# Kernel optimization log

Hardware: AMD Instinct MI355X
Metric: run time of the kernel (lower is better)

## Reference

```python
import jax, jax.numpy as jnp
import numpy as np

N_NODES = 1048576
N_SEG = 16384
NODES_PER_SEG = N_NODES // N_SEG
D = 128
EPS = 1e-5


def setup_inputs() -> dict:
    key = jax.random.key(0)
    ks = jax.random.split(key, 8)
    feat = jax.random.normal(ks[0], (N_NODES, D), dtype=jnp.float32)
    position_weight = jax.random.uniform(ks[1], (N_NODES,), dtype=jnp.float32)
    # equal-size segments (sessions): contiguous, sorted segment ids
    segment_ids = jnp.repeat(jnp.arange(N_SEG, dtype=jnp.int32), NODES_PER_SEG)
    # last node of each segment
    last_nodes = jnp.arange(N_SEG, dtype=jnp.int32) * NODES_PER_SEG + (NODES_PER_SEG - 1)
    # parameters
    gamma = jnp.ones((D,), dtype=jnp.float32)
    beta = jnp.zeros((D,), dtype=jnp.float32)
    s = 1.0 / np.sqrt(D)
    W_u = jax.random.uniform(ks[2], (D, D), dtype=jnp.float32, minval=-s, maxval=s)
    W_i = jax.random.uniform(ks[3], (D, D), dtype=jnp.float32, minval=-s, maxval=s)
    b_i = jax.random.uniform(ks[4], (D,), dtype=jnp.float32, minval=-s, maxval=s)
    w_e = jax.random.uniform(ks[5], (D,), dtype=jnp.float32, minval=-s, maxval=s)
    return {
        "feat": feat, "position_weight": position_weight,
        "last_nodes": last_nodes, "segment_ids": segment_ids,
        "gamma": gamma, "beta": beta, "W_u": W_u, "W_i": W_i,
        "b_i": b_i, "w_e": w_e, "num_segments": N_SEG,
    }


def reference(feat, position_weight, last_nodes, segment_ids, gamma, beta,
              W_u, W_i, b_i, w_e, num_segments):
    # BatchNorm1d (training-mode batch statistics)
    mean = feat.mean(axis=0)
    var = jnp.mean((feat - mean) ** 2, axis=0)
    f = (feat - mean) * (gamma / jnp.sqrt(var + EPS)) + beta  # [N, D]

    feat_u = f @ W_u.T                                         # [N, H]
    feat_last = f[last_nodes] @ W_i.T + b_i                    # [B, H]
    # broadcast_nodes: gather per-graph vector back to its nodes
    e = jax.nn.sigmoid(feat_u + feat_last[segment_ids]) @ w_e  # [N]

    # segment softmax over nodes of each graph
    m = jax.ops.segment_max(e, segment_ids, num_segments=num_segments)
    ex = jnp.exp(e - m[segment_ids])
    denom = jax.ops.segment_sum(ex, segment_ids, num_segments=num_segments)
    alpha = ex / denom[segment_ids]                            # [N]

    rst = jax.ops.segment_sum(f * alpha[:, None], segment_ids,
                              num_segments=num_segments)       # [B, D]
    position_rst = jax.ops.segment_sum(f * position_weight[:, None], segment_ids,
                                       num_segments=num_segments)  # [B, D]
    return rst, position_rst
```

## Files before the change

### kernel.cpp

```cpp
#include <hip/hip_runtime.h>

#define N_NODES 1048576
#define N_SEG   16384
#define NPS     64
#define D       128
#define EPS     1e-5f

typedef float f4 __attribute__((ext_vector_type(4)));
typedef float f32x4 __attribute__((ext_vector_type(4)));
typedef __bf16 bf16x8 __attribute__((ext_vector_type(8)));
typedef unsigned u32x4 __attribute__((ext_vector_type(4)));

__global__ __launch_bounds__(256) void k_stats(const float* __restrict__ feat,
                                               float* __restrict__ part) {
    int t = threadIdx.x;
    long gid = (long)blockIdx.x * 256 + t;
    const f4* f4p = (const f4*)feat;
    f4 s = {0.f,0.f,0.f,0.f}, q = {0.f,0.f,0.f,0.f};
#pragma unroll 8
    for (int k = 0; k < 64; ++k) {
        f4 v = f4p[gid + (long)k * 524288];
        s += v;
        q += v * v;
    }
    __shared__ f4 red[2][8][32];
    red[0][t >> 5][t & 31] = s;
    red[1][t >> 5][t & 31] = q;
    __syncthreads();
    int stat = t >> 7, c = t & 127;
    const float* base = (const float*)&red[stat][0][0];
    float acc = 0.f;
#pragma unroll
    for (int r = 0; r < 8; ++r) acc += base[r * 128 + c];
    part[(stat * 128 + c) * 2048 + blockIdx.x] = acc;
}

__global__ __launch_bounds__(256) void k_scale(const float* __restrict__ part,
                                               const float* __restrict__ gamma,
                                               const float* __restrict__ beta,
                                               float* __restrict__ scl,
                                               float* __restrict__ shf) {
    int t = threadIdx.x, c = blockIdx.x;
    float s1 = 0.f, s2 = 0.f;
#pragma unroll
    for (int j = 0; j < 8; ++j) {
        s1 += part[c * 2048 + t + 256 * j];
        s2 += part[(128 + c) * 2048 + t + 256 * j];
    }
    __shared__ float rs[256], rq[256];
    rs[t] = s1; rq[t] = s2;
    __syncthreads();
    for (int off = 128; off > 0; off >>= 1) {
        if (t < off) { rs[t] += rs[t + off]; rq[t] += rq[t + off]; }
        __syncthreads();
    }
    if (t == 0) {
        float mean = rs[0] / (float)N_NODES;
        float var  = rq[0] / (float)N_NODES - mean * mean;
        float sc   = gamma[c] * rsqrtf(var + EPS);
        scl[c] = sc;
        shf[c] = beta[c] - mean * sc;
    }
}

__device__ inline unsigned pk2(float x, float y) {
    unsigned a = __builtin_bit_cast(unsigned, x);
    unsigned b = __builtin_bit_cast(unsigned, y);
    a = (a + 0x7fffu + ((a >> 16) & 1u)) >> 16;
    b = (b + 0x7fffu + ((b >> 16) & 1u)) & 0xffff0000u;
    return a | b;
}
__device__ inline bf16x8 lds8(const unsigned short* p, int row, int kb) {
    int addr = (row * 256 + kb) ^ ((row & 7) << 4);
    return *(const bf16x8*)((const char*)p + addr);
}
__device__ inline bf16x8 bfrag(const float* __restrict__ W, int h, int kk, int g4) {
    const float* p = W + h * 128 + kk * 32 + g4 * 8;
    f4 u = *(const f4*)p;
    f4 v = *(const f4*)(p + 4);
    u32x4 r = { pk2(u.x, u.y), pk2(u.z, u.w), pk2(v.x, v.y), pk2(v.z, v.w) };
    return __builtin_bit_cast(bf16x8, r);
}
__device__ inline void bar_lgkm() {
    asm volatile("s_waitcnt lgkmcnt(0)" ::: "memory");
    __builtin_amdgcn_s_barrier();
    __builtin_amdgcn_sched_barrier(0);
}
__device__ inline void bar_vm1() {
    asm volatile("s_waitcnt vmcnt(1) lgkmcnt(0)" ::: "memory");
    __builtin_amdgcn_s_barrier();
    __builtin_amdgcn_sched_barrier(0);
}
__device__ inline void bar_vm0() {
    asm volatile("s_waitcnt vmcnt(0) lgkmcnt(0)" ::: "memory");
    __builtin_amdgcn_s_barrier();
    __builtin_amdgcn_sched_barrier(0);
}
__device__ inline void stage_tile(const float* __restrict__ segbase, float* fbuf,
                                  int w, int lane) {
#pragma unroll
    for (int j = 0; j < 8; ++j) {
        int chunk = w * 8 + j;
        int p = (chunk << 10) + lane * 16;
        int g = p ^ (((p >> 9) & 7) << 4);
        __builtin_amdgcn_global_load_lds(
            (const __attribute__((address_space(1))) void*)((const char*)segbase + g),
            (__attribute__((address_space(3))) void*)((char*)fbuf + (chunk << 10)),
            16, 0, 0);
    }
}

__global__ __launch_bounds__(256, 2) void k_main(const float* __restrict__ feat,
                                                 const float* __restrict__ pw,
                                                 const float* __restrict__ Wu,
                                                 const float* __restrict__ Wi,
                                                 const float* __restrict__ bi,
                                                 const float* __restrict__ we,
                                                 const float* __restrict__ scl,
                                                 const float* __restrict__ shf,
                                                 float* __restrict__ out) {
    __shared__ __align__(16) float fbuf[64 * 128];
    __shared__ __align__(16) unsigned short abuf[64 * 128];
    __shared__ float flp_s[8][128];
    __shared__ float pw_s[512];
    __shared__ float epart[4][64];
    __shared__ float wpR[4][128];
    __shared__ float wpP[4][128];

    int t = threadIdx.x;
    int lane = t & 63, w = t >> 6;
    int l15 = lane & 15, g4 = lane >> 4;
    int c0 = 4 * (t & 31);
    f4 vscl = *(const f4*)(scl + c0);
    f4 vshf = *(const f4*)(shf + c0);
    int h_a = l15 + 32 * w;
    int h_b = h_a + 16;
    int seg0 = blockIdx.x * 8;

    stage_tile(feat + (long)seg0 * NPS * D, fbuf, w, lane);
    pw_s[t] = pw[seg0 * NPS + t];
    pw_s[t + 256] = pw[seg0 * NPS + t + 256];
    {
        int r = t >> 5;
        long row = (long)(seg0 + r) * NPS + (NPS - 1);
        f4 v = *(const f4*)(feat + row * 128 + c0);
        v = v * vscl + vshf;
        int addr = (r * 256 + 8 * (t & 31)) ^ ((r & 7) << 4);
        *(uint2*)((char*)abuf + addr) = make_uint2(pk2(v.x, v.y), pk2(v.z, v.w));
        int r2 = r + 8;
        int addr2 = (r2 * 256 + 8 * (t & 31)) ^ ((r2 & 7) << 4);
        *(uint2*)((char*)abuf + addr2) = make_uint2(0u, 0u);
    }
    bar_lgkm();
    {
        f32x4 a2[2];
        a2[0] = (f32x4){0.f,0.f,0.f,0.f};
        a2[1] = (f32x4){0.f,0.f,0.f,0.f};
#pragma unroll
        for (int kk = 0; kk < 4; ++kk) {
            bf16x8 a = lds8(abuf, l15, kk * 64 + g4 * 16);
            a2[0] = __builtin_amdgcn_mfma_f32_16x16x32_bf16(a, bfrag(Wi, h_a, kk, g4), a2[0], 0, 0, 0);
            a2[1] = __builtin_amdgcn_mfma_f32_16x16x32_bf16(a, bfrag(Wi, h_b, kk, g4), a2[1], 0, 0, 0);
        }
        float bia = bi[h_a], bib = bi[h_b];
#pragma unroll
        for (int r = 0; r < 4; ++r) {
            int si = 4 * g4 + r;
            if (si < 8) {
                flp_s[si][h_a] = a2[0][r] + bia;
                flp_s[si][h_b] = a2[1][r] + bib;
            }
        }
    }
    bf16x8 bW[8];
#pragma unroll
    for (int kk = 0; kk < 4; ++kk) {
        bW[kk]     = bfrag(Wu, h_a, kk, g4);
        bW[4 + kk] = bfrag(Wu, h_b, kk, g4);
    }
    float we0 = we[h_a], we1 = we[h_b];
    bar_vm0();

    for (int it = 0; it < 8; ++it) {
        int seg = seg0 + it;
#pragma unroll
        for (int k = 0; k < 8; ++k) {
            int n = (t >> 5) + 8 * k;
            int q = (n * 512 + 16 * (t & 31)) ^ ((n & 7) << 4);
            f4 v = *(const f4*)((const char*)fbuf + q);
            v = v * vscl + vshf;
            int addr = (n * 256 + 8 * (t & 31)) ^ ((n & 7) << 4);
            *(uint2*)((char*)abuf + addr) = make_uint2(pk2(v.x, v.y), pk2(v.z, v.w));
        }
        bar_lgkm();
        if (it < 7)
            stage_tile(feat + (long)(seg + 1) * NPS * D, fbuf, w, lane);

        float fl0 = flp_s[it][h_a];
        float fl1 = flp_s[it][h_b];
        f32x4 acc[4][2];
#pragma unroll
        for (int nf = 0; nf < 4; ++nf) {
            acc[nf][0] = (f32x4){0.f,0.f,0.f,0.f};
            acc[nf][1] = (f32x4){0.f,0.f,0.f,0.f};
        }
#pragma unroll
        for (int kk = 0; kk < 4; ++kk) {
            int kb = kk * 64 + g4 * 16;
            bf16x8 a[4];
#pragma unroll
            for (int nf = 0; nf < 4; ++nf) a[nf] = lds8(abuf, l15 + 16 * nf, kb);
#pragma unroll
            for (int nf = 0; nf < 4; ++nf) {
                acc[nf][0] = __builtin_amdgcn_mfma_f32_16x16x32_bf16(a[nf], bW[kk],     acc[nf][0], 0, 0, 0);
                acc[nf][1] = __builtin_amdgcn_mfma_f32_16x16x32_bf16(a[nf], bW[4 + kk], acc[nf][1], 0, 0, 0);
            }
        }
#pragma unroll
        for (int nf = 0; nf < 4; ++nf) {
#pragma unroll
            for (int r = 0; r < 4; ++r) {
                float x0 = acc[nf][0][r] + fl0;
                float x1 = acc[nf][1][r] + fl1;
                float p = we0 / (1.f + __expf(-x0)) + we1 / (1.f + __expf(-x1));
                p += __shfl_xor(p, 1);
                p += __shfl_xor(p, 2);
                p += __shfl_xor(p, 4);
                p += __shfl_xor(p, 8);
                if (l15 == 0) epart[w][16 * nf + 4 * g4 + r] = p;
            }
        }
        bar_lgkm();

        float e = epart[0][lane] + epart[1][lane] + epart[2][lane] + epart[3][lane];
        float m = e;
#pragma unroll
        for (int off = 32; off > 0; off >>= 1) m = fmaxf(m, __shfl_xor(m, off));
        float ex = __expf(e - m);
        float sd = ex;
#pragma unroll
        for (int off = 32; off > 0; off >>= 1) sd += __shfl_xor(sd, off);
        float al = ex / sd;

        f4 racc = {0.f,0.f,0.f,0.f}, pacc = {0.f,0.f,0.f,0.f};
#pragma unroll
        for (int k = 0; k < 8; ++k) {
            int n = (t >> 5) + 8 * k;
            int addr = (n * 256 + 8 * (t & 31)) ^ ((n & 7) << 4);
            uint2 u = *(const uint2*)((const char*)abuf + addr);
            f4 fv;
            fv.x = __builtin_bit_cast(float, u.x << 16);
            fv.y = __builtin_bit_cast(float, u.x & 0xffff0000u);
            fv.z = __builtin_bit_cast(float, u.y << 16);
            fv.w = __builtin_bit_cast(float, u.y & 0xffff0000u);
            float av = __shfl(al, n);
            float pv = pw_s[it * NPS + n];
            racc += av * fv;
            pacc += pv * fv;
        }
#pragma unroll
        for (int c = 0; c < 4; ++c) {
            racc[c] += __shfl_xor(racc[c], 32);
            pacc[c] += __shfl_xor(pacc[c], 32);
        }
        if (lane < 32) {
            *(f4*)&wpR[w][4 * lane] = racc;
            *(f4*)&wpP[w][4 * lane] = pacc;
        }
        bar_lgkm();

        if (t < 128) {
            out[(long)seg * 128 + t] = wpR[0][t] + wpR[1][t] + wpR[2][t] + wpR[3][t];
        } else {
            int c = t - 128;
            out[(long)N_SEG * 128 + (long)seg * 128 + c] =
                wpP[0][c] + wpP[1][c] + wpP[2][c] + wpP[3][c];
        }
        bar_vm1();
    }
}

extern "C" void kernel_launch(void* const* d_in, const int* in_sizes, int n_in,
                              void* d_out, int out_size, void* d_ws, size_t ws_size,
                              hipStream_t stream) {
    const float* feat       = (const float*)d_in[0];
    const float* pw         = (const float*)d_in[1];
    const float* gamma      = (const float*)d_in[4];
    const float* beta       = (const float*)d_in[5];
    const float* Wu         = (const float*)d_in[6];
    const float* Wi         = (const float*)d_in[7];
    const float* bi         = (const float*)d_in[8];
    const float* we         = (const float*)d_in[9];
    float* out = (float*)d_out;

    float* ws   = (float*)d_ws;
    float* part = ws;
    float* wscl = ws + 524288;
    float* wshf = ws + 524288 + 128;

    k_stats<<<dim3(2048), dim3(256), 0, stream>>>(feat, part);
    k_scale<<<dim3(128),  dim3(256), 0, stream>>>(part, gamma, beta, wscl, wshf);
    k_main <<<dim3(2048), dim3(256), 0, stream>>>(feat, pw, Wu, Wi, bi, we, wscl, wshf, out);
}
```

Measured before the change: 359.9 us.

## Prefetch next segment tile into registers instead of async global-to-LDS staging

Replaces the global_load_lds staging of each 64x128 fp32 segment tile into a shared buffer with direct register prefetch: each thread loads 8 float4 values for the next segment while the current one is computed, then normalizes and packs them into the bf16 LDS tile. This removes the 32KB fp32 LDS buffer and its read-back, lowering LDS traffic and footprint, and drops the vmcnt-based barriers. In exchange it raises VGPR pressure by 32 registers, which may limit occupancy under launch_bounds(256,2), and the loads' latency is hidden only by the compiler's waitcnt placement.

```diff
diff --git a/kernel.cpp b/kernel.cpp
--- a/kernel.cpp
+++ b/kernel.cpp
@@ -82,32 +82,10 @@
     return __builtin_bit_cast(bf16x8, r);
 }
 __device__ inline void bar_lgkm() {
+    __builtin_amdgcn_sched_barrier(0);
     asm volatile("s_waitcnt lgkmcnt(0)" ::: "memory");
     __builtin_amdgcn_s_barrier();
     __builtin_amdgcn_sched_barrier(0);
-}
-__device__ inline void bar_vm1() {
-    asm volatile("s_waitcnt vmcnt(1) lgkmcnt(0)" ::: "memory");
-    __builtin_amdgcn_s_barrier();
-    __builtin_amdgcn_sched_barrier(0);
-}
-__device__ inline void bar_vm0() {
-    asm volatile("s_waitcnt vmcnt(0) lgkmcnt(0)" ::: "memory");
-    __builtin_amdgcn_s_barrier();
-    __builtin_amdgcn_sched_barrier(0);
-}
-__device__ inline void stage_tile(const float* __restrict__ segbase, float* fbuf,
-                                  int w, int lane) {
-#pragma unroll
-    for (int j = 0; j < 8; ++j) {
-        int chunk = w * 8 + j;
-        int p = (chunk << 10) + lane * 16;
-        int g = p ^ (((p >> 9) & 7) << 4);
-        __builtin_amdgcn_global_load_lds(
-            (const __attribute__((address_space(1))) void*)((const char*)segbase + g),
-            (__attribute__((address_space(3))) void*)((char*)fbuf + (chunk << 10)),
-            16, 0, 0);
-    }
 }
 
 __global__ __launch_bounds__(256, 2) void k_main(const float* __restrict__ feat,
@@ -119,7 +97,6 @@
                                                  const float* __restrict__ scl,
                                                  const float* __restrict__ shf,
                                                  float* __restrict__ out) {
-    __shared__ __align__(16) float fbuf[64 * 128];
     __shared__ __align__(16) unsigned short abuf[64 * 128];
     __shared__ float flp_s[8][128];
     __shared__ float pw_s[512];
@@ -137,7 +114,14 @@
     int h_b = h_a + 16;
     int seg0 = blockIdx.x * 8;
 
-    stage_tile(feat + (long)seg0 * NPS * D, fbuf, w, lane);
+    f4 fn[8];
+    {
+        const f4* src = (const f4*)(feat + (long)seg0 * NPS * D);
+#pragma unroll
+        for (int k = 0; k < 8; ++k) fn[k] = src[t + 256 * k];
+    }
+    __builtin_amdgcn_sched_barrier(0);
+
     pw_s[t] = pw[seg0 * NPS + t];
     pw_s[t + 256] = pw[seg0 * NPS + t + 256];
     {
@@ -179,22 +163,24 @@
         bW[4 + kk] = bfrag(Wu, h_b, kk, g4);
     }
     float we0 = we[h_a], we1 = we[h_b];
-    bar_vm0();
+    bar_lgkm();
 
     for (int it = 0; it < 8; ++it) {
         int seg = seg0 + it;
 #pragma unroll
         for (int k = 0; k < 8; ++k) {
+            f4 v = fn[k] * vscl + vshf;
             int n = (t >> 5) + 8 * k;
-            int q = (n * 512 + 16 * (t & 31)) ^ ((n & 7) << 4);
-            f4 v = *(const f4*)((const char*)fbuf + q);
-            v = v * vscl + vshf;
             int addr = (n * 256 + 8 * (t & 31)) ^ ((n & 7) << 4);
             *(uint2*)((char*)abuf + addr) = make_uint2(pk2(v.x, v.y), pk2(v.z, v.w));
         }
         bar_lgkm();
-        if (it < 7)
-            stage_tile(feat + (long)(seg + 1) * NPS * D, fbuf, w, lane);
+        if (it < 7) {
+            const f4* src = (const f4*)(feat + (long)(seg + 1) * NPS * D);
+#pragma unroll
+            for (int k = 0; k < 8; ++k) fn[k] = src[t + 256 * k];
+        }
+        __builtin_amdgcn_sched_barrier(0);
 
         float fl0 = flp_s[it][h_a];
         float fl1 = flp_s[it][h_b];
@@ -276,7 +262,6 @@
             out[(long)N_SEG * 128 + (long)seg * 128 + c] =
                 wpP[0][c] + wpP[1][c] + wpP[2][c] + wpP[3][c];
         }
-        bar_vm1();
     }
 }
 
```

After: 359.2 us. No clear change (-0.2%).
